# Optimization experiments

Hardware: AMD Instinct MI355X
Metric: run time of the kernel (lower is better)

Reference implementation:

```python
import jax, jax.numpy as jnp
import numpy as np

B, S, D = 2, 2048, 1024
H = 16
HD = D // H

def setup_inputs() -> dict:
    key = jax.random.key(0)
    k1, k2, k3 = jax.random.split(key, 3)
    x = jax.random.normal(k1, (B, S, D), dtype=jnp.float32)
    w_attn = jax.random.normal(k2, (D, 3 * D), dtype=jnp.float32) * (1.0 / np.sqrt(D))
    b_attn = jnp.zeros((3 * D,), dtype=jnp.float32)
    w_proj = jax.random.normal(k3, (D, D), dtype=jnp.float32) * (1.0 / np.sqrt(D))
    b_proj = jnp.zeros((D,), dtype=jnp.float32)
    return {"x": x, "w_attn": w_attn, "b_attn": b_attn, "w_proj": w_proj, "b_proj": b_proj}

def reference(x, w_attn, b_attn, w_proj, b_proj):
    bsz, seq_len, embed_dim = x.shape
    qkv = x @ w_attn + b_attn                      # [B,S,3D]
    q, k, v = jnp.split(qkv, 3, axis=-1)
    # [B,S,D] -> [B,H,S,HD]
    def heads(t):
        return t.reshape(bsz, seq_len, H, HD).transpose(0, 2, 1, 3)
    q, k, v = heads(q), heads(k), heads(v)
    scale = 1.0 / np.sqrt(HD)
    att = jnp.einsum('bhqd,bhkd->bhqk', q, k) * scale  # [B,H,S,S]
    causal = jnp.tril(jnp.ones((seq_len, seq_len), dtype=bool))
    att = jnp.where(causal[None, None], att, jnp.float32(-jnp.inf))
    att = jax.nn.softmax(att, axis=-1)
    y = jnp.einsum('bhqk,bhkd->bhqd', att, v)          # [B,H,S,HD]
    y = y.transpose(0, 2, 1, 3).reshape(bsz, seq_len, embed_dim)
    return y @ w_proj + b_proj
```

## Files before the change

kernel.cpp:

```cpp
#include <hip/hip_runtime.h>
#include <hip/hip_bf16.h>
#include <math.h>

typedef __bf16 bf16x8 __attribute__((ext_vector_type(8)));
typedef __bf16 bf16x4 __attribute__((ext_vector_type(4)));
typedef float f32x4 __attribute__((ext_vector_type(4)));

#define LOG2E 1.44269504088896340736f

#define SEQ 2048
#define DMODEL 1024
#define NH 16
#define HD 64

__device__ __forceinline__ void gl2lds16(const void* g, void* l) {
  __builtin_amdgcn_global_load_lds((__attribute__((address_space(1))) void*)g,
                                   (__attribute__((address_space(3))) void*)l,
                                   16, 0, 0);
}

__global__ void detect_dtype(const unsigned* __restrict__ x, unsigned* __restrict__ flag) {
  __shared__ int cnt[256];
  int c = 0;
  for (int i = threadIdx.x; i < 4096; i += 256) {
    unsigned e = (x[i] >> 23) & 0xFF;
    c += (e >= 0x70 && e <= 0x8F) ? 1 : 0;
  }
  cnt[threadIdx.x] = c;
  __syncthreads();
  for (int s = 128; s > 0; s >>= 1) {
    if ((int)threadIdx.x < s) cnt[threadIdx.x] += cnt[threadIdx.x + s];
    __syncthreads();
  }
  if (threadIdx.x == 0) flag[0] = (cnt[0] > 2048) ? 1u : 0u;
}

__global__ void conv_to_bf16(const void* __restrict__ in, __hip_bfloat16* __restrict__ out,
                             int n, const unsigned* __restrict__ flag) {
  const int i = (blockIdx.x * 256 + threadIdx.x) * 4;
  if (i >= n) return;
  if (*flag) {
    const float4 v = *(const float4*)((const float*)in + i);
    out[i + 0] = __float2bfloat16(v.x);
    out[i + 1] = __float2bfloat16(v.y);
    out[i + 2] = __float2bfloat16(v.z);
    out[i + 3] = __float2bfloat16(v.w);
  } else {
    const __hip_bfloat16* bin = (const __hip_bfloat16*)in;
    out[i + 0] = bin[i + 0];
    out[i + 1] = bin[i + 1];
    out[i + 2] = bin[i + 2];
    out[i + 3] = bin[i + 3];
  }
}

__global__ void transpose_cvt(const void* __restrict__ in, __hip_bfloat16* __restrict__ out,
                              int R, int C, const unsigned* __restrict__ flag) {
  __shared__ __hip_bfloat16 tile[64][65];
  const bool f32 = (*flag != 0);
  const int c0 = blockIdx.x * 64, r0 = blockIdx.y * 64;
  const int tx = threadIdx.x & 63, ty = threadIdx.x >> 6;
#pragma unroll
  for (int i = 0; i < 16; ++i) {
    int r = ty + i * 4;
    long idx = (long)(r0 + r) * C + c0 + tx;
    tile[r][tx] = f32 ? __float2bfloat16(((const float*)in)[idx])
                      : ((const __hip_bfloat16*)in)[idx];
  }
  __syncthreads();
#pragma unroll
  for (int i = 0; i < 16; ++i) {
    int r = ty + i * 4;
    out[(long)(c0 + r) * R + r0 + tx] = tile[tx][r];
  }
}

template <int MODE>
__global__ __launch_bounds__(256, 2) void gemm_bt(
    const __hip_bfloat16* __restrict__ A, const __hip_bfloat16* __restrict__ Bt,
    const __hip_bfloat16* __restrict__ bias, void* __restrict__ C,
    __hip_bfloat16* __restrict__ q_ws, __hip_bfloat16* __restrict__ k_ws,
    __hip_bfloat16* __restrict__ vt_ws, int M, int N, int K,
    const unsigned* __restrict__ flag) {
  alignas(16) __shared__ __hip_bfloat16 lA[128 * 32];
  alignas(16) __shared__ __hip_bfloat16 lB[128 * 32];
  const int tid = threadIdx.x;
  const int wave = tid >> 6, lane = tid & 63;
  const int l15 = lane & 15, lq = lane >> 4;
  const int m0 = blockIdx.y * 128, n0 = blockIdx.x * 128;
  const int wrow = (wave >> 1) * 64, wcol = (wave & 1) * 64;

  const int cg = (lane & 3) ^ ((lane >> 3) & 3);
  const __hip_bfloat16* ap0 = A + (long)(m0 + wave * 16 + (lane >> 2)) * K + cg * 8;
  const __hip_bfloat16* bp0 = Bt + (long)(n0 + wave * 16 + (lane >> 2)) * K + cg * 8;
  __hip_bfloat16* lA0 = lA + wave * 512;
  __hip_bfloat16* lA1 = lA + (wave + 4) * 512;
  __hip_bfloat16* lB0 = lB + wave * 512;
  __hip_bfloat16* lB1 = lB + (wave + 4) * 512;

  f32x4 acc[4][4];
#pragma unroll
  for (int i = 0; i < 4; ++i)
#pragma unroll
    for (int j = 0; j < 4; ++j) acc[i][j] = {0.f, 0.f, 0.f, 0.f};

  const int fc = (lq ^ ((l15 >> 1) & 3)) * 8;

  for (int k0 = 0; k0 < K; k0 += 32) {
    __syncthreads();
    gl2lds16(ap0 + k0, lA0);
    gl2lds16(ap0 + (long)64 * K + k0, lA1);
    gl2lds16(bp0 + k0, lB0);
    gl2lds16(bp0 + (long)64 * K + k0, lB1);
    __syncthreads();
    bf16x8 af[4], bfr[4];
#pragma unroll
    for (int i = 0; i < 4; ++i)
      af[i] = *(const bf16x8*)(lA + (wrow + 16 * i + l15) * 32 + fc);
#pragma unroll
    for (int j = 0; j < 4; ++j)
      bfr[j] = *(const bf16x8*)(lB + (wcol + 16 * j + l15) * 32 + fc);
#pragma unroll
    for (int i = 0; i < 4; ++i)
#pragma unroll
      for (int j = 0; j < 4; ++j)
        acc[i][j] = __builtin_amdgcn_mfma_f32_16x16x32_bf16(af[i], bfr[j], acc[i][j], 0, 0, 0);
  }

  const bool outf32 = (MODE == 0) && (*flag != 0);
  const float KSCL = 0.125f * LOG2E;
#pragma unroll
  for (int i = 0; i < 4; ++i) {
    const int row = m0 + wrow + 16 * i + lq * 4;
#pragma unroll
    for (int j = 0; j < 4; ++j) {
      const int col = n0 + wcol + 16 * j + l15;
      const float bv = __bfloat162float(bias[col]);
#pragma unroll
      for (int r = 0; r < 4; ++r) {
        const float v = acc[i][j][r] + bv;
        const int rr = row + r;
        if (MODE == 0) {
          if (outf32)
            ((float*)C)[(long)rr * N + col] = v;
          else
            ((__hip_bfloat16*)C)[(long)rr * N + col] = __float2bfloat16(v);
        } else {
          const int which = col >> 10;
          const int f = col & 1023;
          const int h = f >> 6, d = f & 63;
          const int b = rr >> 11, s = rr & 2047;
          const long bh = (long)b * NH + h;
          if (which == 0)
            q_ws[(bh * SEQ + s) * HD + d] = __float2bfloat16(v);
          else if (which == 1)
            k_ws[(bh * SEQ + s) * HD + d] = __float2bfloat16(v * KSCL);
          else {
            const int w = s & 31;
            const int wl = w & 15;
            const int sig = (w >> 4) ? (2 * (wl & ~3) + 4 + (wl & 3))
                                     : (2 * (wl & ~3) + (wl & 3));
            const int sp = (s & ~31) | sig;
            vt_ws[(bh * HD + d) * SEQ + sp] = __float2bfloat16(v);
          }
        }
      }
    }
  }
}

__global__ __launch_bounds__(256, 4) void attn_fused(
    const __hip_bfloat16* __restrict__ q_ws, const __hip_bfloat16* __restrict__ k_ws,
    const __hip_bfloat16* __restrict__ vt_ws, __hip_bfloat16* __restrict__ y_ws) {
  alignas(16) __shared__ __hip_bfloat16 lK[2][64 * 64];
  alignas(16) __shared__ __hip_bfloat16 lV[2][64 * 64];
  const int tid = threadIdx.x, wave = tid >> 6, lane = tid & 63;
  const int l15 = lane & 15, lq = lane >> 4;
  const int qt = 31 - (blockIdx.x >> 5);
  const int bh = blockIdx.x & 31;
  const int q0 = qt * 64;
  const int nkt = qt + 1;
  const __hip_bfloat16* Qb = q_ws + (long)bh * SEQ * HD;
  const __hip_bfloat16* Kb = k_ws + (long)bh * SEQ * HD;
  const __hip_bfloat16* Vb = vt_ws + (long)bh * HD * SEQ;
  const int b = bh >> 4, h = bh & 15;

  const int qrow = q0 + wave * 16 + l15;
  const bf16x8 qa0 = *(const bf16x8*)(Qb + (long)qrow * HD + lq * 8);
  const bf16x8 qa1 = *(const bf16x8*)(Qb + (long)qrow * HD + 32 + lq * 8);

  f32x4 accO[4];
  f32x4 accL;
#pragma unroll
  for (int j = 0; j < 4; ++j) accO[j] = {0.f, 0.f, 0.f, 0.f};
  accL = {0.f, 0.f, 0.f, 0.f};
  const __bf16 one = (__bf16)1.0f;
  const bf16x8 onesA = {one, one, one, one, one, one, one, one};

  const int p0 = wave * 16 + (lane >> 3);
  const int cl = lane & 7;

#pragma unroll
  for (int i = 0; i < 2; ++i) {
    const int p = p0 + i * 8;
    const int c = cl ^ (p & 7);
    gl2lds16(Kb + (long)p * HD + c * 8, &lK[0][(wave * 16 + i * 8) * 64]);
    gl2lds16(Vb + (long)p * SEQ + c * 8, &lV[0][(wave * 16 + i * 8) * 64]);
  }
  __syncthreads();

#pragma unroll 1
  for (int kt = 0; kt < nkt; ++kt) {
    const int buf = kt & 1;
    if (kt + 1 < nkt) {
      const int kb = (kt + 1) * 64;
#pragma unroll
      for (int i = 0; i < 2; ++i) {
        const int p = p0 + i * 8;
        const int c = cl ^ (p & 7);
        gl2lds16(Kb + (long)(kb + p) * HD + c * 8, &lK[buf ^ 1][(wave * 16 + i * 8) * 64]);
        gl2lds16(Vb + (long)p * SEQ + kb + c * 8, &lV[buf ^ 1][(wave * 16 + i * 8) * 64]);
      }
    }
    const __hip_bfloat16* lKb = lK[buf];
    const __hip_bfloat16* lVb = lV[buf];

    f32x4 st[4];
#pragma unroll
    for (int t = 0; t < 4; ++t) {
      st[t] = {0.f, 0.f, 0.f, 0.f};
      const int pp = t * 16 + l15;
      const bf16x8 kb0 = *(const bf16x8*)(lKb + (pp * 8 + (lq ^ (pp & 7))) * 8);
      const bf16x8 kb1 = *(const bf16x8*)(lKb + (pp * 8 + ((4 + lq) ^ (pp & 7))) * 8);
      st[t] = __builtin_amdgcn_mfma_f32_16x16x32_bf16(kb0, qa0, st[t], 0, 0, 0);
      st[t] = __builtin_amdgcn_mfma_f32_16x16x32_bf16(kb1, qa1, st[t], 0, 0, 0);
    }

    const bool diag = (kt == nkt - 1);
    const int qloc = wave * 16 + l15;
    bf16x8 pb[2];
#pragma unroll
    for (int c = 0; c < 2; ++c) {
#pragma unroll
      for (int t2 = 0; t2 < 2; ++t2) {
        const int tt = c * 2 + t2;
#pragma unroll
        for (int r = 0; r < 4; ++r) {
          float pv = exp2f(st[tt][r]);
          if (diag) {
            const int colloc = tt * 16 + lq * 4 + r;
            pv = (colloc <= qloc) ? pv : 0.f;
          }
          pb[c][t2 * 4 + r] = (__bf16)pv;
        }
      }
    }

#pragma unroll
    for (int j = 0; j < 4; ++j) {
      const int d = j * 16 + l15;
      const bf16x8 va0 = *(const bf16x8*)(lVb + (d * 8 + (lq ^ (d & 7))) * 8);
      const bf16x8 va1 = *(const bf16x8*)(lVb + (d * 8 + ((4 + lq) ^ (d & 7))) * 8);
      accO[j] = __builtin_amdgcn_mfma_f32_16x16x32_bf16(va0, pb[0], accO[j], 0, 0, 0);
      accO[j] = __builtin_amdgcn_mfma_f32_16x16x32_bf16(va1, pb[1], accO[j], 0, 0, 0);
    }
    accL = __builtin_amdgcn_mfma_f32_16x16x32_bf16(onesA, pb[0], accL, 0, 0, 0);
    accL = __builtin_amdgcn_mfma_f32_16x16x32_bf16(onesA, pb[1], accL, 0, 0, 0);
    __syncthreads();
  }

  const float inv = 1.f / accL[0];
  const int s = q0 + wave * 16 + l15;
  __hip_bfloat16* yb = y_ws + (long)(b * SEQ + s) * DMODEL + h * HD;
#pragma unroll
  for (int j = 0; j < 4; ++j) {
    bf16x4 o;
#pragma unroll
    for (int r = 0; r < 4; ++r) o[r] = (__bf16)(accO[j][r] * inv);
    *(bf16x4*)(yb + j * 16 + lq * 4) = o;
  }
}

extern "C" void kernel_launch(void* const* d_in, const int* in_sizes, int n_in,
                              void* d_out, int out_size, void* d_ws, size_t ws_size,
                              hipStream_t stream) {
  const void* x = d_in[0];
  const void* w_attn = d_in[1];
  const void* b_attn = d_in[2];
  const void* w_proj = d_in[3];
  const void* b_proj = d_in[4];

  char* ws = (char*)d_ws;
  const size_t MB = 1024 * 1024;
  unsigned* flag = (unsigned*)ws;
  __hip_bfloat16* wT_attn = (__hip_bfloat16*)(ws + 1 * MB);
  __hip_bfloat16* wT_proj = (__hip_bfloat16*)(ws + 7 * MB);
  __hip_bfloat16* x_bf = (__hip_bfloat16*)(ws + 9 * MB);
  __hip_bfloat16* q_ws = (__hip_bfloat16*)(ws + 17 * MB);
  __hip_bfloat16* k_ws = (__hip_bfloat16*)(ws + 25 * MB);
  __hip_bfloat16* vt_ws = (__hip_bfloat16*)(ws + 33 * MB);
  __hip_bfloat16* y_ws = (__hip_bfloat16*)(ws + 41 * MB);
  __hip_bfloat16* bA_bf = (__hip_bfloat16*)(ws + 49 * MB);
  __hip_bfloat16* bP_bf = (__hip_bfloat16*)(ws + 49 * MB + 8192);

  detect_dtype<<<1, 256, 0, stream>>>((const unsigned*)x, flag);

  conv_to_bf16<<<4096, 256, 0, stream>>>(x, x_bf, 4194304, flag);
  conv_to_bf16<<<3, 256, 0, stream>>>(b_attn, bA_bf, 3072, flag);
  conv_to_bf16<<<1, 256, 0, stream>>>(b_proj, bP_bf, 1024, flag);
  transpose_cvt<<<dim3(3072 / 64, 1024 / 64), 256, 0, stream>>>(w_attn, wT_attn, 1024, 3072, flag);
  transpose_cvt<<<dim3(1024 / 64, 1024 / 64), 256, 0, stream>>>(w_proj, wT_proj, 1024, 1024, flag);

  gemm_bt<1><<<dim3(3072 / 128, 4096 / 128), 256, 0, stream>>>(
      x_bf, wT_attn, bA_bf, nullptr, q_ws, k_ws, vt_ws, 4096, 3072, 1024, flag);

  attn_fused<<<dim3(1024), 256, 0, stream>>>(q_ws, k_ws, vt_ws, y_ws);

  gemm_bt<0><<<dim3(1024 / 128, 4096 / 128), 256, 0, stream>>>(
      y_ws, wT_proj, bP_bf, d_out, nullptr, nullptr, nullptr, 4096, 1024, 1024, flag);
}
```

Baseline: 206.5 us.

## Process 128 query rows per attention block to reuse K/V tiles

Each attention block now handles a 128-row query tile, with every wave computing two 16-row groups, so each K/V tile loaded into LDS feeds twice as many MFMAs. The grid halves to 512 blocks, and the tile order is reordered so heavy and light causal tiles interleave for better balance. The causal mask now covers the last two key tiles using global column indices. Launch bounds change as well: attention drops to 2 blocks per SM and the GEMM rises to 3, which trades occupancy against the larger register footprint.

```diff
diff --git a/kernel.cpp b/kernel.cpp
--- a/kernel.cpp
+++ b/kernel.cpp
@@ -76,7 +76,7 @@
 }
 
 template <int MODE>
-__global__ __launch_bounds__(256, 2) void gemm_bt(
+__global__ __launch_bounds__(256, 3) void gemm_bt(
     const __hip_bfloat16* __restrict__ A, const __hip_bfloat16* __restrict__ Bt,
     const __hip_bfloat16* __restrict__ bias, void* __restrict__ C,
     __hip_bfloat16* __restrict__ q_ws, __hip_bfloat16* __restrict__ k_ws,
@@ -169,31 +169,39 @@
   }
 }
 
-__global__ __launch_bounds__(256, 4) void attn_fused(
+__global__ __launch_bounds__(256, 2) void attn_fused(
     const __hip_bfloat16* __restrict__ q_ws, const __hip_bfloat16* __restrict__ k_ws,
     const __hip_bfloat16* __restrict__ vt_ws, __hip_bfloat16* __restrict__ y_ws) {
   alignas(16) __shared__ __hip_bfloat16 lK[2][64 * 64];
   alignas(16) __shared__ __hip_bfloat16 lV[2][64 * 64];
   const int tid = threadIdx.x, wave = tid >> 6, lane = tid & 63;
   const int l15 = lane & 15, lq = lane >> 4;
-  const int qt = 31 - (blockIdx.x >> 5);
+  const int idx = blockIdx.x >> 5;
+  const int qt = (idx < 8) ? (15 - idx) : (idx - 8);
   const int bh = blockIdx.x & 31;
-  const int q0 = qt * 64;
-  const int nkt = qt + 1;
+  const int q0 = qt * 128;
+  const int nkt = 2 * qt + 2;
   const __hip_bfloat16* Qb = q_ws + (long)bh * SEQ * HD;
   const __hip_bfloat16* Kb = k_ws + (long)bh * SEQ * HD;
   const __hip_bfloat16* Vb = vt_ws + (long)bh * HD * SEQ;
   const int b = bh >> 4, h = bh & 15;
 
-  const int qrow = q0 + wave * 16 + l15;
-  const bf16x8 qa0 = *(const bf16x8*)(Qb + (long)qrow * HD + lq * 8);
-  const bf16x8 qa1 = *(const bf16x8*)(Qb + (long)qrow * HD + 32 + lq * 8);
-
-  f32x4 accO[4];
-  f32x4 accL;
-#pragma unroll
-  for (int j = 0; j < 4; ++j) accO[j] = {0.f, 0.f, 0.f, 0.f};
-  accL = {0.f, 0.f, 0.f, 0.f};
+  bf16x8 qa[2][2];
+#pragma unroll
+  for (int g = 0; g < 2; ++g) {
+    const int qrow = q0 + wave * 32 + g * 16 + l15;
+    qa[g][0] = *(const bf16x8*)(Qb + (long)qrow * HD + lq * 8);
+    qa[g][1] = *(const bf16x8*)(Qb + (long)qrow * HD + 32 + lq * 8);
+  }
+
+  f32x4 accO[2][4];
+  f32x4 accL[2];
+#pragma unroll
+  for (int g = 0; g < 2; ++g) {
+#pragma unroll
+    for (int j = 0; j < 4; ++j) accO[g][j] = {0.f, 0.f, 0.f, 0.f};
+    accL[g] = {0.f, 0.f, 0.f, 0.f};
+  }
   const __bf16 one = (__bf16)1.0f;
   const bf16x8 onesA = {one, one, one, one, one, one, one, one};
 
@@ -225,33 +233,40 @@
     const __hip_bfloat16* lKb = lK[buf];
     const __hip_bfloat16* lVb = lV[buf];
 
-    f32x4 st[4];
+    f32x4 st[2][4];
 #pragma unroll
     for (int t = 0; t < 4; ++t) {
-      st[t] = {0.f, 0.f, 0.f, 0.f};
       const int pp = t * 16 + l15;
       const bf16x8 kb0 = *(const bf16x8*)(lKb + (pp * 8 + (lq ^ (pp & 7))) * 8);
       const bf16x8 kb1 = *(const bf16x8*)(lKb + (pp * 8 + ((4 + lq) ^ (pp & 7))) * 8);
-      st[t] = __builtin_amdgcn_mfma_f32_16x16x32_bf16(kb0, qa0, st[t], 0, 0, 0);
-      st[t] = __builtin_amdgcn_mfma_f32_16x16x32_bf16(kb1, qa1, st[t], 0, 0, 0);
-    }
-
-    const bool diag = (kt == nkt - 1);
-    const int qloc = wave * 16 + l15;
-    bf16x8 pb[2];
-#pragma unroll
-    for (int c = 0; c < 2; ++c) {
-#pragma unroll
-      for (int t2 = 0; t2 < 2; ++t2) {
-        const int tt = c * 2 + t2;
-#pragma unroll
-        for (int r = 0; r < 4; ++r) {
-          float pv = exp2f(st[tt][r]);
-          if (diag) {
-            const int colloc = tt * 16 + lq * 4 + r;
-            pv = (colloc <= qloc) ? pv : 0.f;
+#pragma unroll
+      for (int g = 0; g < 2; ++g) {
+        f32x4 z = {0.f, 0.f, 0.f, 0.f};
+        z = __builtin_amdgcn_mfma_f32_16x16x32_bf16(kb0, qa[g][0], z, 0, 0, 0);
+        st[g][t] = __builtin_amdgcn_mfma_f32_16x16x32_bf16(kb1, qa[g][1], z, 0, 0, 0);
+      }
+    }
+
+    const bool diag = (kt >= nkt - 2);
+    const int colbase = kt * 64;
+    bf16x8 pb[2][2];
+#pragma unroll
+    for (int g = 0; g < 2; ++g) {
+      const int qglob = q0 + wave * 32 + g * 16 + l15;
+#pragma unroll
+      for (int c = 0; c < 2; ++c) {
+#pragma unroll
+        for (int t2 = 0; t2 < 2; ++t2) {
+          const int tt = c * 2 + t2;
+#pragma unroll
+          for (int r = 0; r < 4; ++r) {
+            float pv = exp2f(st[g][tt][r]);
+            if (diag) {
+              const int col = colbase + tt * 16 + lq * 4 + r;
+              pv = (col <= qglob) ? pv : 0.f;
+            }
+            pb[g][c][t2 * 4 + r] = (__bf16)pv;
           }
-          pb[c][t2 * 4 + r] = (__bf16)pv;
         }
       }
     }
@@ -261,23 +276,32 @@
       const int d = j * 16 + l15;
       const bf16x8 va0 = *(const bf16x8*)(lVb + (d * 8 + (lq ^ (d & 7))) * 8);
       const bf16x8 va1 = *(const bf16x8*)(lVb + (d * 8 + ((4 + lq) ^ (d & 7))) * 8);
-      accO[j] = __builtin_amdgcn_mfma_f32_16x16x32_bf16(va0, pb[0], accO[j], 0, 0, 0);
-      accO[j] = __builtin_amdgcn_mfma_f32_16x16x32_bf16(va1, pb[1], accO[j], 0, 0, 0);
-    }
-    accL = __builtin_amdgcn_mfma_f32_16x16x32_bf16(onesA, pb[0], accL, 0, 0, 0);
-    accL = __builtin_amdgcn_mfma_f32_16x16x32_bf16(onesA, pb[1], accL, 0, 0, 0);
+#pragma unroll
+      for (int g = 0; g < 2; ++g) {
+        accO[g][j] = __builtin_amdgcn_mfma_f32_16x16x32_bf16(va0, pb[g][0], accO[g][j], 0, 0, 0);
+        accO[g][j] = __builtin_amdgcn_mfma_f32_16x16x32_bf16(va1, pb[g][1], accO[g][j], 0, 0, 0);
+      }
+    }
+#pragma unroll
+    for (int g = 0; g < 2; ++g) {
+      accL[g] = __builtin_amdgcn_mfma_f32_16x16x32_bf16(onesA, pb[g][0], accL[g], 0, 0, 0);
+      accL[g] = __builtin_amdgcn_mfma_f32_16x16x32_bf16(onesA, pb[g][1], accL[g], 0, 0, 0);
+    }
     __syncthreads();
   }
 
-  const float inv = 1.f / accL[0];
-  const int s = q0 + wave * 16 + l15;
-  __hip_bfloat16* yb = y_ws + (long)(b * SEQ + s) * DMODEL + h * HD;
-#pragma unroll
-  for (int j = 0; j < 4; ++j) {
-    bf16x4 o;
-#pragma unroll
-    for (int r = 0; r < 4; ++r) o[r] = (__bf16)(accO[j][r] * inv);
-    *(bf16x4*)(yb + j * 16 + lq * 4) = o;
+#pragma unroll
+  for (int g = 0; g < 2; ++g) {
+    const float inv = 1.f / accL[g][0];
+    const int s = q0 + wave * 32 + g * 16 + l15;
+    __hip_bfloat16* yb = y_ws + (long)(b * SEQ + s) * DMODEL + h * HD;
+#pragma unroll
+    for (int j = 0; j < 4; ++j) {
+      bf16x4 o;
+#pragma unroll
+      for (int r = 0; r < 4; ++r) o[r] = (__bf16)(accO[g][j][r] * inv);
+      *(bf16x4*)(yb + j * 16 + lq * 4) = o;
+    }
   }
 }
 
@@ -314,7 +338,7 @@
   gemm_bt<1><<<dim3(3072 / 128, 4096 / 128), 256, 0, stream>>>(
       x_bf, wT_attn, bA_bf, nullptr, q_ws, k_ws, vt_ws, 4096, 3072, 1024, flag);
 
-  attn_fused<<<dim3(1024), 256, 0, stream>>>(q_ws, k_ws, vt_ws, y_ws);
+  attn_fused<<<dim3(512), 256, 0, stream>>>(q_ws, k_ws, vt_ws, y_ws);
 
   gemm_bt<0><<<dim3(1024 / 128, 4096 / 128), 256, 0, stream>>>(
       y_ws, wT_proj, bP_bf, d_out, nullptr, nullptr, nullptr, 4096, 1024, 1024, flag);
```

Result: slower. 226.5 us (+9.7%).
